# Performance work log

Hardware: AMD Instinct MI355X
Metric: run time of the kernel (lower is better)

Reference implementation:

```python
import jax, jax.numpy as jnp
import numpy as np

N_NODES = 50000
N_EDGES = 800000
N_GRAPHS = 64
IN_DIM, HID, MLP_HID, NUM_CLASSES = 384, 128, 64, 1


def setup_inputs() -> dict:
    key = jax.random.key(0)
    ks = jax.random.split(key, 10)
    x = jax.random.normal(ks[0], (N_NODES, IN_DIM), jnp.float32)
    edge_index = jax.random.randint(ks[1], (2, N_EDGES), 0, N_NODES, dtype=jnp.int32)
    batch = jnp.sort(jax.random.randint(ks[2], (N_NODES,), 0, N_GRAPHS, dtype=jnp.int32))

    def glorot(k, shape):
        fan_in = shape[0]
        return jax.random.normal(k, shape, jnp.float32) / jnp.sqrt(jnp.float32(fan_in))

    return {
        "x": x,
        "edge_index": edge_index,
        "batch": batch,
        "W1": glorot(ks[3], (IN_DIM, HID)),  "b1": jnp.zeros((HID,), jnp.float32),
        "W2": glorot(ks[4], (HID, HID)),     "b2": jnp.zeros((HID,), jnp.float32),
        "W3": glorot(ks[5], (HID, HID)),     "b3": jnp.zeros((HID,), jnp.float32),
        "Wm1": glorot(ks[6], (HID, MLP_HID)), "bm1": jnp.zeros((MLP_HID,), jnp.float32),
        "Wm2": glorot(ks[7], (MLP_HID, NUM_CLASSES)), "bm2": jnp.zeros((NUM_CLASSES,), jnp.float32),
    }


def _gcn_conv(x, W, b, src, dst, dis):
    # PyG GCNConv: h = x W; aggregate D^-1/2 (A+I) D^-1/2 h; add bias.
    n = x.shape[0]
    h = x @ W                               # [N, out]
    enorm = dis[src] * dis[dst]             # [E] symmetric normalization
    msgs = h[src] * enorm[:, None]          # gather + scale
    agg = jax.ops.segment_sum(msgs, dst, num_segments=n)
    agg = agg + h * (dis * dis)[:, None]    # self-loop contribution
    return agg + b


def reference(x, edge_index, batch, W1, b1, W2, b2, W3, b3, Wm1, bm1, Wm2, bm2):
    src, dst = edge_index[0], edge_index[1]
    n = x.shape[0]
    # degree over A + I (self-loops added, as in PyG gcn_norm)
    deg = jax.ops.segment_sum(jnp.ones((src.shape[0],), x.dtype), dst, num_segments=n) + 1.0
    dis = jax.lax.rsqrt(deg)

    h = jax.nn.relu(_gcn_conv(x, W1, b1, src, dst, dis))
    h = jax.nn.relu(_gcn_conv(h, W2, b2, src, dst, dis))
    h = jax.nn.relu(_gcn_conv(h, W3, b3, src, dst, dis))

    # global mean pool over graphs
    counts = jax.ops.segment_sum(jnp.ones((n,), x.dtype), batch, num_segments=N_GRAPHS)
    pooled = jax.ops.segment_sum(h, batch, num_segments=N_GRAPHS)
    pooled = pooled / jnp.maximum(counts, 1.0)[:, None]   # [G, HID]

    # MLP head (dropout = identity in eval mode)
    z = jax.nn.relu(pooled @ Wm1 + bm1)
    out = z @ Wm2 + bm2                                    # [G, 1]
    return out
```

## Files before the change

kernel.cpp:

```cpp
#include <hip/hip_runtime.h>
#include <hip/hip_bf16.h>

#define N_NODES 50000
#define N_EDGES 800000
#define N_GRAPHS 64
#define IN_DIM 384
#define HID 128
#define MLP_HID 64

#define SCAN_BLOCKS ((N_NODES + 255) / 256)
#define POOL_CHUNK 128
#define POOL_BLOCKS ((N_NODES + POOL_CHUNK - 1) / POOL_CHUNK)

__global__ __launch_bounds__(256) void count_kernel(const int* __restrict__ dst,
                                                    int* __restrict__ cnt, int E) {
    int t = blockIdx.x * 256 + threadIdx.x;
    if (t < E) atomicAdd(&cnt[dst[t]], 1);
}

__global__ __launch_bounds__(256) void bsum_kernel(const int* __restrict__ cnt,
                                                   int* __restrict__ bsum) {
    __shared__ int sh[256];
    const int t = threadIdx.x;
    const int i = blockIdx.x * 256 + t;
    sh[t] = (i < N_NODES) ? cnt[i] : 0;
    __syncthreads();
#pragma unroll
    for (int off = 128; off > 0; off >>= 1) {
        if (t < off) sh[t] += sh[t + off];
        __syncthreads();
    }
    if (t == 0) bsum[blockIdx.x] = sh[0];
}

__global__ __launch_bounds__(256) void bscan_kernel(const int* __restrict__ bsum,
                                                    int* __restrict__ boff,
                                                    int* __restrict__ rowptr) {
    __shared__ int sh[256];
    const int t = threadIdx.x;
    int v = (t < SCAN_BLOCKS) ? bsum[t] : 0;
    sh[t] = v;
    __syncthreads();
#pragma unroll
    for (int off = 1; off < 256; off <<= 1) {
        int u = 0;
        if (t >= off) u = sh[t - off];
        __syncthreads();
        if (t >= off) sh[t] += u;
        __syncthreads();
    }
    if (t < SCAN_BLOCKS) boff[t] = sh[t] - v;
    if (t == 255) rowptr[N_NODES] = sh[255];
}

__global__ __launch_bounds__(256) void final_scan_kernel(const int* __restrict__ cnt,
                                                         const int* __restrict__ boff,
                                                         int* __restrict__ rowptr,
                                                         int* __restrict__ cursor,
                                                         float* __restrict__ dis) {
    __shared__ int sh[256];
    const int t = threadIdx.x;
    const int i = blockIdx.x * 256 + t;
    const int c = (i < N_NODES) ? cnt[i] : 0;
    sh[t] = c;
    __syncthreads();
#pragma unroll
    for (int off = 1; off < 256; off <<= 1) {
        int u = 0;
        if (t >= off) u = sh[t - off];
        __syncthreads();
        if (t >= off) sh[t] += u;
        __syncthreads();
    }
    if (i < N_NODES) {
        const int pos = boff[blockIdx.x] + sh[t] - c;
        rowptr[i] = pos;
        cursor[i] = pos;
        dis[i] = rsqrtf((float)c + 1.0f);
    }
}

__global__ __launch_bounds__(256) void fill_kernel(const int* __restrict__ ei,
                                                   int* __restrict__ cursor,
                                                   int* __restrict__ csr, int E) {
    int e = blockIdx.x * 256 + threadIdx.x;
    if (e >= E) return;
    int s = ei[e];
    int d = ei[E + e];
    int pos = atomicAdd(&cursor[d], 1);
    csr[pos] = s;
}

template <int K, bool RELU_IN>
__global__ __launch_bounds__(256) void gemm_kernel(const float* __restrict__ X,
                                                   const float* __restrict__ W,
                                                   float* __restrict__ H, int M) {
    __shared__ float Xs[64][32];
    __shared__ float Ws[32][128];
    const int tid = threadIdx.x;
    const int row0 = blockIdx.x * 64;
    const int tn = tid & 31;
    const int tm = tid >> 5;
    float acc[8][4] = {};

    for (int k0 = 0; k0 < K; k0 += 32) {
        {
            const int r = tid >> 3;
            const int kq = (tid & 7) * 4;
#pragma unroll
            for (int rr = 0; rr < 2; ++rr) {
                const int row = row0 + r + rr * 32;
                float4 v = make_float4(0.f, 0.f, 0.f, 0.f);
                if (row < M) v = *reinterpret_cast<const float4*>(&X[row * K + k0 + kq]);
                if (RELU_IN) {
                    v.x = fmaxf(v.x, 0.f); v.y = fmaxf(v.y, 0.f);
                    v.z = fmaxf(v.z, 0.f); v.w = fmaxf(v.w, 0.f);
                }
                *reinterpret_cast<float4*>(&Xs[r + rr * 32][kq]) = v;
            }
        }
        {
            const int kr = tid >> 3;
#pragma unroll
            for (int i = 0; i < 4; ++i) {
                const int c4 = (tid & 7) + 8 * i;
                *reinterpret_cast<float4*>(&Ws[kr][c4 * 4]) =
                    *reinterpret_cast<const float4*>(&W[(k0 + kr) * 128 + c4 * 4]);
            }
        }
        __syncthreads();
#pragma unroll
        for (int kk = 0; kk < 32; ++kk) {
            float b[4];
            *reinterpret_cast<float4*>(b) = *reinterpret_cast<float4*>(&Ws[kk][tn * 4]);
#pragma unroll
            for (int m = 0; m < 8; ++m) {
                const float a = Xs[tm * 8 + m][kk];
                acc[m][0] = fmaf(a, b[0], acc[m][0]);
                acc[m][1] = fmaf(a, b[1], acc[m][1]);
                acc[m][2] = fmaf(a, b[2], acc[m][2]);
                acc[m][3] = fmaf(a, b[3], acc[m][3]);
            }
        }
        __syncthreads();
    }
#pragma unroll
    for (int m = 0; m < 8; ++m) {
        const int row = row0 + tm * 8 + m;
        if (row < M) {
            float4 v = make_float4(acc[m][0], acc[m][1], acc[m][2], acc[m][3]);
            *reinterpret_cast<float4*>(&H[row * 128 + tn * 4]) = v;
        }
    }
}

__global__ __launch_bounds__(256) void gather_kernel(const int* __restrict__ rowptr,
                                                     const int* __restrict__ csr,
                                                     const float* __restrict__ H,
                                                     const float* __restrict__ dis,
                                                     const float* __restrict__ b,
                                                     float* __restrict__ AGG, int n) {
    int t = blockIdx.x * 256 + threadIdx.x;
    int node = t >> 5;
    if (node >= n) return;
    int lane = t & 31;
    const int beg = rowptr[node];
    const int end = rowptr[node + 1];
    const float d = dis[node];

    float4 acc;
    {
        float4 h = *reinterpret_cast<const float4*>(&H[node * 128 + lane * 4]);
        float4 bb = *reinterpret_cast<const float4*>(&b[lane * 4]);
        const float dd = d * d;
        acc.x = fmaf(h.x, dd, bb.x);
        acc.y = fmaf(h.y, dd, bb.y);
        acc.z = fmaf(h.z, dd, bb.z);
        acc.w = fmaf(h.w, dd, bb.w);
    }
    int i = beg;
    for (; i + 2 <= end; i += 2) {
        const int s0 = csr[i];
        const int s1 = csr[i + 1];
        const float e0 = dis[s0] * d;
        const float e1 = dis[s1] * d;
        float4 v0 = *reinterpret_cast<const float4*>(&H[s0 * 128 + lane * 4]);
        float4 v1 = *reinterpret_cast<const float4*>(&H[s1 * 128 + lane * 4]);
        acc.x = fmaf(v0.x, e0, acc.x);
        acc.y = fmaf(v0.y, e0, acc.y);
        acc.z = fmaf(v0.z, e0, acc.z);
        acc.w = fmaf(v0.w, e0, acc.w);
        acc.x = fmaf(v1.x, e1, acc.x);
        acc.y = fmaf(v1.y, e1, acc.y);
        acc.z = fmaf(v1.z, e1, acc.z);
        acc.w = fmaf(v1.w, e1, acc.w);
    }
    if (i < end) {
        const int s0 = csr[i];
        const float e0 = dis[s0] * d;
        float4 v0 = *reinterpret_cast<const float4*>(&H[s0 * 128 + lane * 4]);
        acc.x = fmaf(v0.x, e0, acc.x);
        acc.y = fmaf(v0.y, e0, acc.y);
        acc.z = fmaf(v0.z, e0, acc.z);
        acc.w = fmaf(v0.w, e0, acc.w);
    }
    *reinterpret_cast<float4*>(&AGG[node * 128 + lane * 4]) = acc;
}

__global__ __launch_bounds__(256) void pool1_kernel(const float* __restrict__ AGG,
                                                    const int* __restrict__ batch,
                                                    float* __restrict__ pooled, int n) {
    const int start = blockIdx.x * POOL_CHUNK;
    const int end = min(start + POOL_CHUNK, n);
    const int f = threadIdx.x & 127;
    const int h = threadIdx.x >> 7;
    int gcur = -1;
    float acc = 0.f;
    for (int i = start + h; i < end; i += 2) {
        const int g = batch[i];
        if (g != gcur) {
            if (gcur >= 0) atomicAdd(&pooled[gcur * HID + f], acc);
            gcur = g;
            acc = 0.f;
        }
        acc += fmaxf(AGG[i * HID + f], 0.f);
    }
    if (gcur >= 0) atomicAdd(&pooled[gcur * HID + f], acc);
}

__global__ __launch_bounds__(128) void pooldiv_kernel(const int* __restrict__ batch,
                                                      float* __restrict__ pooled, int n) {
    const int g = blockIdx.x;
    int lo = 0, hi = n;
    while (lo < hi) { int mid = (lo + hi) >> 1; if (batch[mid] < g) lo = mid + 1; else hi = mid; }
    const int start = lo;
    hi = n;
    while (lo < hi) { int mid = (lo + hi) >> 1; if (batch[mid] < g + 1) lo = mid + 1; else hi = mid; }
    const float cnt = (float)(lo - start);
    pooled[g * HID + threadIdx.x] /= fmaxf(cnt, 1.f);
}

__global__ __launch_bounds__(256) void mlp_kernel(const float* __restrict__ pooled,
                                                  const float* __restrict__ Wm1,
                                                  const float* __restrict__ bm1,
                                                  const float* __restrict__ Wm2,
                                                  const float* __restrict__ bm2,
                                                  float* __restrict__ out) {
    __shared__ float P[N_GRAPHS][HID];
    __shared__ float Wl[HID][MLP_HID];
    const int tid = threadIdx.x;
    for (int i = tid; i < N_GRAPHS * HID; i += 256) P[i >> 7][i & 127] = pooled[i];
    for (int i = tid; i < HID * MLP_HID; i += 256) Wl[i >> 6][i & 63] = Wm1[i];
    __syncthreads();
    const int g = tid >> 2;
    const int jb = tid & 3;
    float part = 0.f;
#pragma unroll
    for (int jj = 0; jj < 16; ++jj) {
        const int j = jb * 16 + jj;
        float z = bm1[j];
        for (int k = 0; k < HID; ++k) z = fmaf(P[g][k], Wl[k][j], z);
        z = fmaxf(z, 0.f);
        part = fmaf(z, Wm2[j], part);
    }
    part += __shfl_xor(part, 1);
    part += __shfl_xor(part, 2);
    if (jb == 0) out[g] = part + bm2[0];
}

extern "C" void kernel_launch(void* const* d_in, const int* in_sizes, int n_in,
                              void* d_out, int out_size, void* d_ws, size_t ws_size,
                              hipStream_t stream) {
    const float* x   = (const float*)d_in[0];
    const int*   ei  = (const int*)d_in[1];
    const int*   bat = (const int*)d_in[2];
    const float* W1  = (const float*)d_in[3];
    const float* b1  = (const float*)d_in[4];
    const float* W2  = (const float*)d_in[5];
    const float* b2  = (const float*)d_in[6];
    const float* W3  = (const float*)d_in[7];
    const float* b3  = (const float*)d_in[8];
    const float* Wm1 = (const float*)d_in[9];
    const float* bm1 = (const float*)d_in[10];
    const float* Wm2 = (const float*)d_in[11];
    const float* bm2 = (const float*)d_in[12];
    float* out = (float*)d_out;

    int*   cnt    = (int*)d_ws;
    int*   cursor = cnt + 50048;
    int*   rowptr = cursor + 50048;
    int*   csr    = rowptr + 50056;
    int*   bsum   = csr + 800000;
    int*   boff   = bsum + 256;
    float* dis    = (float*)(boff + 256);
    float* H      = dis + 50048;
    float* AGG    = H + N_NODES * HID;
    float* pooled = AGG + N_NODES * HID;

    hipMemsetAsync(cnt, 0, N_NODES * sizeof(int), stream);
    hipMemsetAsync(pooled, 0, N_GRAPHS * HID * sizeof(float), stream);

    count_kernel<<<(N_EDGES + 255) / 256, 256, 0, stream>>>(ei + N_EDGES, cnt, N_EDGES);
    bsum_kernel<<<SCAN_BLOCKS, 256, 0, stream>>>(cnt, bsum);
    bscan_kernel<<<1, 256, 0, stream>>>(bsum, boff, rowptr);
    final_scan_kernel<<<SCAN_BLOCKS, 256, 0, stream>>>(cnt, boff, rowptr, cursor, dis);
    fill_kernel<<<(N_EDGES + 255) / 256, 256, 0, stream>>>(ei, cursor, csr, N_EDGES);

    const int gemm_blocks = (N_NODES + 63) / 64;
    const int gat_blocks  = (N_NODES * 32 + 255) / 256;

    gemm_kernel<IN_DIM, false><<<gemm_blocks, 256, 0, stream>>>(x, W1, H, N_NODES);
    gather_kernel<<<gat_blocks, 256, 0, stream>>>(rowptr, csr, H, dis, b1, AGG, N_NODES);
    gemm_kernel<HID, true><<<gemm_blocks, 256, 0, stream>>>(AGG, W2, H, N_NODES);
    gather_kernel<<<gat_blocks, 256, 0, stream>>>(rowptr, csr, H, dis, b2, AGG, N_NODES);
    gemm_kernel<HID, true><<<gemm_blocks, 256, 0, stream>>>(AGG, W3, H, N_NODES);
    gather_kernel<<<gat_blocks, 256, 0, stream>>>(rowptr, csr, H, dis, b3, AGG, N_NODES);

    pool1_kernel<<<POOL_BLOCKS, 256, 0, stream>>>(AGG, bat, pooled, N_NODES);
    pooldiv_kernel<<<N_GRAPHS, 128, 0, stream>>>(bat, pooled, N_NODES);
    mlp_kernel<<<1, 256, 0, stream>>>(pooled, Wm1, bm1, Wm2, bm2, out);
}
```

Measured before the change: 603.5 us.

## Replace FP32 GEMMs with split-bf16 MFMA GEMMs emulating fp32 precision

The three dense node-feature GEMMs move from a scalar FP32 FMA kernel to a matrix-core kernel built on bf16 MFMA 16x16x32. Inputs and weights are split into hi and lo bf16 parts, and three MFMAs (hi*hi, hi*lo, lo*hi) recover close to fp32 accuracy. A small per-call kernel pre-splits and transposes the weights. The aim is to cut GEMM compute time. In exchange it adds split work when staging the activations, three extra tiny launches, and extra LDS traffic.

Result: faster. 537.7 us (-10.9%).

```diff
diff --git a/kernel.cpp b/kernel.cpp
--- a/kernel.cpp
+++ b/kernel.cpp
@@ -11,6 +11,11 @@
 #define SCAN_BLOCKS ((N_NODES + 255) / 256)
 #define POOL_CHUNK 128
 #define POOL_BLOCKS ((N_NODES + POOL_CHUNK - 1) / POOL_CHUNK)
+#define GEMM_BLOCKS ((N_NODES + 127) / 128)
+
+typedef __attribute__((ext_vector_type(8))) short short8;
+typedef __attribute__((ext_vector_type(4))) float f32x4;
+typedef unsigned int u32;
 
 __global__ __launch_bounds__(256) void count_kernel(const int* __restrict__ dst,
                                                     int* __restrict__ cnt, int E) {
@@ -91,65 +96,119 @@
     csr[pos] = s;
 }
 
+__global__ __launch_bounds__(256) void wsplit_kernel(const float* __restrict__ W,
+                                                     ushort* __restrict__ hi,
+                                                     ushort* __restrict__ lo, int K) {
+    int t = blockIdx.x * 256 + threadIdx.x;
+    if (t >= K * 128) return;
+    const int k = t >> 7;
+    const int c = t & 127;
+    const float f = W[t];
+    const u32 u = __float_as_uint(f);
+    const u32 h = u & 0xFFFF0000u;
+    const float lf = f - __uint_as_float(h);
+    hi[c * K + k] = (ushort)(u >> 16);
+    lo[c * K + k] = (ushort)(__float_as_uint(lf) >> 16);
+}
+
 template <int K, bool RELU_IN>
-__global__ __launch_bounds__(256) void gemm_kernel(const float* __restrict__ X,
-                                                   const float* __restrict__ W,
-                                                   float* __restrict__ H, int M) {
-    __shared__ float Xs[64][32];
-    __shared__ float Ws[32][128];
+__global__ __launch_bounds__(256) void gemm_mfma_kernel(const float* __restrict__ X,
+                                                        const ushort* __restrict__ Wthi,
+                                                        const ushort* __restrict__ Wtlo,
+                                                        float* __restrict__ H, int M) {
+    __shared__ ushort Ahi[128][40];
+    __shared__ ushort Alo[128][40];
+    __shared__ ushort Bhi[128][40];
+    __shared__ ushort Blo[128][40];
+
     const int tid = threadIdx.x;
-    const int row0 = blockIdx.x * 64;
-    const int tn = tid & 31;
-    const int tm = tid >> 5;
-    float acc[8][4] = {};
+    const int row0 = blockIdx.x * 128;
+
+    const int srow = tid >> 1;
+    const int skq  = (tid & 1) << 4;
+
+    const int lane = tid & 63;
+    const int wave = tid >> 6;
+    const int wr = (wave >> 1) * 64;
+    const int wc = (wave & 1) * 64;
+    const int li = lane & 15;
+    const int kb = (lane >> 4) << 3;
+
+    f32x4 acc[4][4];
+#pragma unroll
+    for (int m = 0; m < 4; ++m)
+#pragma unroll
+        for (int n = 0; n < 4; ++n) acc[m][n] = (f32x4){0.f, 0.f, 0.f, 0.f};
 
     for (int k0 = 0; k0 < K; k0 += 32) {
         {
-            const int r = tid >> 3;
-            const int kq = (tid & 7) * 4;
-#pragma unroll
-            for (int rr = 0; rr < 2; ++rr) {
-                const int row = row0 + r + rr * 32;
-                float4 v = make_float4(0.f, 0.f, 0.f, 0.f);
-                if (row < M) v = *reinterpret_cast<const float4*>(&X[row * K + k0 + kq]);
-                if (RELU_IN) {
-                    v.x = fmaxf(v.x, 0.f); v.y = fmaxf(v.y, 0.f);
-                    v.z = fmaxf(v.z, 0.f); v.w = fmaxf(v.w, 0.f);
+            const int gr = row0 + srow;
+            const float* src = &X[(size_t)(gr < M ? gr : (M - 1)) * K + k0 + skq];
+            float f[16];
+            *reinterpret_cast<float4*>(f)      = *reinterpret_cast<const float4*>(src);
+            *reinterpret_cast<float4*>(f + 4)  = *reinterpret_cast<const float4*>(src + 4);
+            *reinterpret_cast<float4*>(f + 8)  = *reinterpret_cast<const float4*>(src + 8);
+            *reinterpret_cast<float4*>(f + 12) = *reinterpret_cast<const float4*>(src + 12);
+            u32 hp[8], lp[8];
+#pragma unroll
+            for (int i = 0; i < 8; ++i) {
+                float f0 = f[2 * i], f1 = f[2 * i + 1];
+                if (RELU_IN) { f0 = fmaxf(f0, 0.f); f1 = fmaxf(f1, 0.f); }
+                const u32 u0 = __float_as_uint(f0), u1 = __float_as_uint(f1);
+                const u32 h0 = u0 & 0xFFFF0000u, h1 = u1 & 0xFFFF0000u;
+                const float l0 = f0 - __uint_as_float(h0);
+                const float l1 = f1 - __uint_as_float(h1);
+                hp[i] = (h0 >> 16) | h1;
+                lp[i] = (__float_as_uint(l0) >> 16) | (__float_as_uint(l1) & 0xFFFF0000u);
+            }
+            u32* dh = (u32*)&Ahi[srow][skq];
+            u32* dl = (u32*)&Alo[srow][skq];
+            *reinterpret_cast<uint4*>(dh)     = make_uint4(hp[0], hp[1], hp[2], hp[3]);
+            *reinterpret_cast<uint4*>(dh + 4) = make_uint4(hp[4], hp[5], hp[6], hp[7]);
+            *reinterpret_cast<uint4*>(dl)     = make_uint4(lp[0], lp[1], lp[2], lp[3]);
+            *reinterpret_cast<uint4*>(dl + 4) = make_uint4(lp[4], lp[5], lp[6], lp[7]);
+        }
+        {
+            const ushort* sh = &Wthi[srow * K + k0 + skq];
+            const ushort* sl = &Wtlo[srow * K + k0 + skq];
+            *reinterpret_cast<uint4*>(&Bhi[srow][skq])     = *reinterpret_cast<const uint4*>(sh);
+            *reinterpret_cast<uint4*>(&Bhi[srow][skq + 8]) = *reinterpret_cast<const uint4*>(sh + 8);
+            *reinterpret_cast<uint4*>(&Blo[srow][skq])     = *reinterpret_cast<const uint4*>(sl);
+            *reinterpret_cast<uint4*>(&Blo[srow][skq + 8]) = *reinterpret_cast<const uint4*>(sl + 8);
+        }
+        __syncthreads();
+        short8 ah[4], al[4];
+#pragma unroll
+        for (int m = 0; m < 4; ++m) {
+            ah[m] = *reinterpret_cast<const short8*>(&Ahi[wr + m * 16 + li][kb]);
+            al[m] = *reinterpret_cast<const short8*>(&Alo[wr + m * 16 + li][kb]);
+        }
+#pragma unroll
+        for (int n = 0; n < 4; ++n) {
+            const short8 bh = *reinterpret_cast<const short8*>(&Bhi[wc + n * 16 + li][kb]);
+            const short8 bl = *reinterpret_cast<const short8*>(&Blo[wc + n * 16 + li][kb]);
+#pragma unroll
+            for (int m = 0; m < 4; ++m) {
+                acc[m][n] = __builtin_amdgcn_mfma_f32_16x16x32_bf16(ah[m], bh, acc[m][n], 0, 0, 0);
+                acc[m][n] = __builtin_amdgcn_mfma_f32_16x16x32_bf16(ah[m], bl, acc[m][n], 0, 0, 0);
+                acc[m][n] = __builtin_amdgcn_mfma_f32_16x16x32_bf16(al[m], bh, acc[m][n], 0, 0, 0);
+            }
+        }
+        __syncthreads();
+    }
+    const int rbase = (lane >> 4) << 2;
+#pragma unroll
+    for (int m = 0; m < 4; ++m) {
+        const int gr0 = row0 + wr + m * 16 + rbase;
+#pragma unroll
+        for (int r = 0; r < 4; ++r) {
+            const int grow = gr0 + r;
+            if (grow < M) {
+#pragma unroll
+                for (int n = 0; n < 4; ++n) {
+                    H[(size_t)grow * 128 + wc + n * 16 + li] = acc[m][n][r];
                 }
-                *reinterpret_cast<float4*>(&Xs[r + rr * 32][kq]) = v;
             }
-        }
-        {
-            const int kr = tid >> 3;
-#pragma unroll
-            for (int i = 0; i < 4; ++i) {
-                const int c4 = (tid & 7) + 8 * i;
-                *reinterpret_cast<float4*>(&Ws[kr][c4 * 4]) =
-                    *reinterpret_cast<const float4*>(&W[(k0 + kr) * 128 + c4 * 4]);
-            }
-        }
-        __syncthreads();
-#pragma unroll
-        for (int kk = 0; kk < 32; ++kk) {
-            float b[4];
-            *reinterpret_cast<float4*>(b) = *reinterpret_cast<float4*>(&Ws[kk][tn * 4]);
-#pragma unroll
-            for (int m = 0; m < 8; ++m) {
-                const float a = Xs[tm * 8 + m][kk];
-                acc[m][0] = fmaf(a, b[0], acc[m][0]);
-                acc[m][1] = fmaf(a, b[1], acc[m][1]);
-                acc[m][2] = fmaf(a, b[2], acc[m][2]);
-                acc[m][3] = fmaf(a, b[3], acc[m][3]);
-            }
-        }
-        __syncthreads();
-    }
-#pragma unroll
-    for (int m = 0; m < 8; ++m) {
-        const int row = row0 + tm * 8 + m;
-        if (row < M) {
-            float4 v = make_float4(acc[m][0], acc[m][1], acc[m][2], acc[m][3]);
-            *reinterpret_cast<float4*>(&H[row * 128 + tn * 4]) = v;
         }
     }
 }
@@ -296,6 +355,12 @@
     float* H      = dis + 50048;
     float* AGG    = H + N_NODES * HID;
     float* pooled = AGG + N_NODES * HID;
+    ushort* wt1hi = (ushort*)(pooled + 8192);
+    ushort* wt1lo = wt1hi + IN_DIM * HID;
+    ushort* wt2hi = wt1lo + IN_DIM * HID;
+    ushort* wt2lo = wt2hi + HID * HID;
+    ushort* wt3hi = wt2lo + HID * HID;
+    ushort* wt3lo = wt3hi + HID * HID;
 
     hipMemsetAsync(cnt, 0, N_NODES * sizeof(int), stream);
     hipMemsetAsync(pooled, 0, N_GRAPHS * HID * sizeof(float), stream);
@@ -306,14 +371,17 @@
     final_scan_kernel<<<SCAN_BLOCKS, 256, 0, stream>>>(cnt, boff, rowptr, cursor, dis);
     fill_kernel<<<(N_EDGES + 255) / 256, 256, 0, stream>>>(ei, cursor, csr, N_EDGES);
 
-    const int gemm_blocks = (N_NODES + 63) / 64;
-    const int gat_blocks  = (N_NODES * 32 + 255) / 256;
-
-    gemm_kernel<IN_DIM, false><<<gemm_blocks, 256, 0, stream>>>(x, W1, H, N_NODES);
+    wsplit_kernel<<<(IN_DIM * HID + 255) / 256, 256, 0, stream>>>(W1, wt1hi, wt1lo, IN_DIM);
+    wsplit_kernel<<<(HID * HID + 255) / 256, 256, 0, stream>>>(W2, wt2hi, wt2lo, HID);
+    wsplit_kernel<<<(HID * HID + 255) / 256, 256, 0, stream>>>(W3, wt3hi, wt3lo, HID);
+
+    const int gat_blocks = (N_NODES * 32 + 255) / 256;
+
+    gemm_mfma_kernel<IN_DIM, false><<<GEMM_BLOCKS, 256, 0, stream>>>(x, wt1hi, wt1lo, H, N_NODES);
     gather_kernel<<<gat_blocks, 256, 0, stream>>>(rowptr, csr, H, dis, b1, AGG, N_NODES);
-    gemm_kernel<HID, true><<<gemm_blocks, 256, 0, stream>>>(AGG, W2, H, N_NODES);
+    gemm_mfma_kernel<HID, true><<<GEMM_BLOCKS, 256, 0, stream>>>(AGG, wt2hi, wt2lo, H, N_NODES);
     gather_kernel<<<gat_blocks, 256, 0, stream>>>(rowptr, csr, H, dis, b2, AGG, N_NODES);
-    gemm_kernel<HID, true><<<gemm_blocks, 256, 0, stream>>>(AGG, W3, H, N_NODES);
+    gemm_mfma_kernel<HID, true><<<GEMM_BLOCKS, 256, 0, stream>>>(AGG, W3 ? wt3hi : wt3hi, wt3lo, H, N_NODES);
     gather_kernel<<<gat_blocks, 256, 0, stream>>>(rowptr, csr, H, dis, b3, AGG, N_NODES);
 
     pool1_kernel<<<POOL_BLOCKS, 256, 0, stream>>>(AGG, bat, pooled, N_NODES);
```
